# Kernel tuning notes

Measured on AMD Instinct MI355X. Metric: run time of the kernel, lower is better.

The kernel has to match this reference:

```python
import jax, jax.numpy as jnp
import numpy as np

N_NODES = 10000
N_EDGES = 320000
IN_FEATS = 500
CONV_DIMS = [500, 256, 256]
FC_DIMS = [256, 128, 40]
BN_EPS = 1e-5


def setup_inputs() -> dict:
    key = jax.random.key(0)
    ks = jax.random.split(key, 16)
    inp = {
        "x": jax.random.normal(ks[0], (N_NODES, IN_FEATS), dtype=jnp.float32),
        "edge_index": jax.random.randint(ks[1], (2, N_EDGES), 0, N_NODES, dtype=jnp.int64),
    }
    # conv layer params: Linear W [in,out], b [out]; BatchNorm gamma/beta [out]
    ki = 2
    for li in range(len(CONV_DIMS) - 1):
        d_in, d_out = CONV_DIMS[li], CONV_DIMS[li + 1]
        s = 1.0 / np.sqrt(d_in)
        inp[f"conv_W{li}"] = jax.random.uniform(ks[ki], (d_in, d_out), jnp.float32, -s, s); ki += 1
        inp[f"conv_b{li}"] = jax.random.uniform(ks[ki], (d_out,), jnp.float32, -s, s); ki += 1
        inp[f"bn_g{li}"] = jnp.ones((d_out,), jnp.float32)
        inp[f"bn_b{li}"] = jnp.zeros((d_out,), jnp.float32)
    for li in range(len(FC_DIMS) - 1):
        d_in, d_out = FC_DIMS[li], FC_DIMS[li + 1]
        s = 1.0 / np.sqrt(d_in)
        inp[f"fc_W{li}"] = jax.random.uniform(ks[ki], (d_in, d_out), jnp.float32, -s, s); ki += 1
        inp[f"fc_b{li}"] = jax.random.uniform(ks[ki], (d_out,), jnp.float32, -s, s); ki += 1
    return inp


def _degree(edge_index, n, dtype):
    # Faithful to: A = eye(N); A[i,j] = 1 per edge (set semantics dedupes repeats).
    A = jnp.eye(n, dtype=dtype).at[edge_index[0], edge_index[1]].set(1.0)
    return A.sum(axis=1)  # deg_i = rowsum of A


def _batchnorm(h, g, b):
    # training-mode BatchNorm1d: batch stats, biased variance
    mean = h.mean(axis=0)
    var = h.var(axis=0)
    return (h - mean) * jax.lax.rsqrt(var + BN_EPS) * g + b


def reference(x, edge_index, conv_W0, conv_b0, bn_g0, bn_b0,
              conv_W1, conv_b1, bn_g1, bn_b1,
              fc_W0, fc_b0, fc_W1, fc_b1):
    n = x.shape[0]
    deg = _degree(edge_index, n, x.dtype)
    # D = sqrt(diag(deg)) is a diagonal matrix, so elementwise D*A*D = diag(deg);
    # mm(D*A*D, x) == deg[:, None] * x (exactly the original math).
    h = x
    for W, b, g, beta in ((conv_W0, conv_b0, bn_g0, bn_b0),
                          (conv_W1, conv_b1, bn_g1, bn_b1)):
        h = (deg[:, None] * h) @ W + b
        h = jax.nn.relu(h)
        h = _batchnorm(h, g, beta)
        # dropout: identity at inference
    for W, b in ((fc_W0, fc_b0), (fc_W1, fc_b1)):
        h = jax.nn.relu(h @ W + b)  # original appends ReLU after every fc, incl. last
    return h
```

## Files before the change

kernel.cpp:

```cpp
#include <hip/hip_runtime.h>

#define NN 10000
#define NE 320000
#define ROW_WORDS 320
#define MP 10112
#define BN_EPS 1e-5f

typedef __attribute__((ext_vector_type(8))) short short8;
typedef __attribute__((ext_vector_type(4))) float f32x4;
typedef unsigned short u16;

__device__ __forceinline__ void split1(float v, u16& h, u16& l) {
    unsigned int u = __float_as_uint(v);
    h = (u16)(u >> 16);
    float hf = __uint_as_float(u & 0xFFFF0000u);
    l = (u16)(__float_as_uint(v - hf) >> 16);
}

__device__ __forceinline__ void gll16(const void* g, void* l) {
    __builtin_amdgcn_global_load_lds(
        (const __attribute__((address_space(1))) unsigned int*)g,
        (__attribute__((address_space(3))) unsigned int*)l, 16, 0, 0);
}

__global__ void scatter_bits(const int* __restrict__ ei, unsigned int* __restrict__ bitmap) {
    int t = blockIdx.x * blockDim.x + threadIdx.x;
    if (t < NE) {
        int i = ei[t];
        int j = ei[NE + t];
        atomicOr(&bitmap[i * ROW_WORDS + (j >> 5)], 1u << (j & 31));
    } else if (t < NE + NN) {
        int i = t - NE;
        atomicOr(&bitmap[i * ROW_WORDS + (i >> 5)], 1u << (i & 31));
    }
}

__device__ void splitW_dev(const float* __restrict__ W, int K, int N, int Kp, int Np,
                           u16* __restrict__ Wt, int bx, int by, char* smem) {
    float (*tile)[65] = (float(*)[65])smem;
    int t = threadIdx.x;
    int bk = bx * 64, bn = by * 64;
    #pragma unroll
    for (int p = 0; p < 4; ++p) {
        int kk = (t >> 4) + p * 16;
        int nc = (t & 15) * 4;
        int k = bk + kk;
        float4 v = {0.f, 0.f, 0.f, 0.f};
        if (k < K && bn + nc + 3 < N)
            v = *(const float4*)&W[(size_t)k * N + bn + nc];
        tile[kk][nc] = v.x; tile[kk][nc + 1] = v.y;
        tile[kk][nc + 2] = v.z; tile[kk][nc + 3] = v.w;
    }
    __syncthreads();
    int nn = t >> 2;
    int kk0 = (t & 3) * 16;
    u16 hs[16], ls[16];
    #pragma unroll
    for (int j = 0; j < 16; ++j) split1(tile[kk0 + j][nn], hs[j], ls[j]);
    size_t ob = (size_t)(bn + nn) * Kp + bk + kk0;
    size_t lo = (size_t)Np * Kp;
    *(short8*)&Wt[ob] = *(short8*)hs;
    *(short8*)&Wt[ob + 8] = *(short8*)&hs[8];
    *(short8*)&Wt[lo + ob] = *(short8*)ls;
    *(short8*)&Wt[lo + ob + 8] = *(short8*)&ls[8];
}

__device__ void xsplit_dev(const float* __restrict__ x, u16* __restrict__ xs, int gblk) {
    int t = threadIdx.x;
    int r0 = gblk * 16 + (t >> 4);
    int l = t & 15;
    u16* xlo = xs + (size_t)MP * 512;
    #pragma unroll
    for (int j = 0; j < 8; ++j) {
        int k = (l + j * 16) * 4;
        float vals[4] = {0.f, 0.f, 0.f, 0.f};
        if (r0 < NN && k < 500) {
            float4 v = *(const float4*)&x[(size_t)r0 * 500 + k];
            vals[0] = v.x; vals[1] = v.y; vals[2] = v.z; vals[3] = v.w;
        }
        ushort4 hs, ls;
        split1(vals[0], hs.x, ls.x); split1(vals[1], hs.y, ls.y);
        split1(vals[2], hs.z, ls.z); split1(vals[3], hs.w, ls.w);
        *(ushort4*)&xs[(size_t)r0 * 512 + k] = hs;
        *(ushort4*)&xlo[(size_t)r0 * 512 + k] = ls;
    }
}

__device__ void degree_dev(const unsigned int* __restrict__ bitmap, float* __restrict__ deg,
                           int gblk) {
    int t = threadIdx.x;
    int r = gblk * 16 + (t >> 4), l = t & 15;
    int cnt = 0;
    if (r < NN)
        for (int wd = l; wd < ROW_WORDS; wd += 16)
            cnt += __popc(bitmap[(size_t)r * ROW_WORDS + wd]);
    cnt += __shfl_down(cnt, 8, 16);
    cnt += __shfl_down(cnt, 4, 16);
    cnt += __shfl_down(cnt, 2, 16);
    cnt += __shfl_down(cnt, 1, 16);
    if (l == 0 && r < NN) deg[r] = (float)cnt;
}

__global__ __launch_bounds__(256)
void prep(const unsigned int* __restrict__ bitmap, const float* __restrict__ x,
          const float* __restrict__ W0, const float* __restrict__ fW1,
          float* __restrict__ deg, u16* __restrict__ xs,
          u16* __restrict__ W0t, u16* __restrict__ fW1t) {
    __shared__ char smem[16704];
    int b = blockIdx.x;
    if (b < 632) {
        degree_dev(bitmap, deg, b);
        xsplit_dev(x, xs, b);
    } else if (b < 664) {
        int idx = b - 632;
        splitW_dev(W0, 500, 256, 512, 256, W0t, idx & 7, idx >> 3, smem);
    } else {
        splitW_dev(fW1, 128, 40, 128, 64, fW1t, b - 664, 0, smem);
    }
}

__global__ __launch_bounds__(256, 4)
void conv0_gemm(const u16* __restrict__ Ahi, const u16* __restrict__ Alo,
                const u16* __restrict__ Bhi, const u16* __restrict__ Blo,
                const float* __restrict__ bias, const float* __restrict__ deg,
                float* __restrict__ stats, u16* __restrict__ Ohi, u16* __restrict__ Olo) {
    __shared__ char smem[32768];
    const int Kp = 512, M = NN, No = 256;
    const int b = blockIdx.x;
    const int xcd = b & 7, g = b >> 3;
    const int bx = g & 3, by = (g >> 2) * 8 + xcd;
    if (by >= 158) return;
    const int t = threadIdx.x;
    const int lane = t & 63;
    const int w = t >> 6;
    const int q = lane >> 4;
    const int l16 = lane & 15;
    const int m7 = l16 & 7;
    const int row0 = by * 64;
    const int col0 = bx * 64;

    const u16* bases[4] = {Ahi, Alo, Bhi, Blo};
    const u16* srcs[8];
    unsigned dstoff[8];
    #pragma unroll
    for (int i = 0; i < 8; ++i) {
        int gi = w + i * 4;
        int reg = i >> 1;
        int j = gi & 7;
        int rb = (reg < 2) ? row0 : col0;
        int r = j * 8 + (lane >> 3);
        int c = (lane & 7) ^ (r & 7);
        srcs[i] = bases[reg] + (size_t)(rb + r) * Kp + c * 8;
        dstoff[i] = reg * 8192 + j * 1024;
    }

    f32x4 acc[4];
    #pragma unroll
    for (int s = 0; s < 4; ++s) acc[s] = (f32x4){0.f, 0.f, 0.f, 0.f};

    #pragma unroll
    for (int i = 0; i < 8; ++i) { gll16(srcs[i], smem + dstoff[i]); srcs[i] += 64; }

    for (int k0 = 0; k0 < Kp; k0 += 64) {
        __syncthreads();
        short8 ah[2], al[2], bh[2][4], bl[2][4];
        #pragma unroll
        for (int kc = 0; kc < 2; ++kc) {
            int aoff = (w * 16 + l16) * 128 + (((kc * 4 + q) ^ m7) * 16);
            ah[kc] = *(const short8*)(smem + aoff);
            al[kc] = *(const short8*)(smem + 8192 + aoff);
            #pragma unroll
            for (int s = 0; s < 4; ++s) {
                int boff = (s * 16 + l16) * 128 + (((kc * 4 + q) ^ m7) * 16);
                bh[kc][s] = *(const short8*)(smem + 16384 + boff);
                bl[kc][s] = *(const short8*)(smem + 24576 + boff);
            }
        }
        __syncthreads();
        if (k0 + 64 < Kp) {
            #pragma unroll
            for (int i = 0; i < 8; ++i) { gll16(srcs[i], smem + dstoff[i]); srcs[i] += 64; }
        }
        #pragma unroll
        for (int kc = 0; kc < 2; ++kc)
            #pragma unroll
            for (int s = 0; s < 4; ++s) {
                acc[s] = __builtin_amdgcn_mfma_f32_16x16x32_bf16(al[kc], bh[kc][s], acc[s], 0, 0, 0);
                acc[s] = __builtin_amdgcn_mfma_f32_16x16x32_bf16(ah[kc], bl[kc][s], acc[s], 0, 0, 0);
                acc[s] = __builtin_amdgcn_mfma_f32_16x16x32_bf16(ah[kc], bh[kc][s], acc[s], 0, 0, 0);
            }
    }

    int growb = row0 + w * 16 + q * 4;
    float dgv[4];
    #pragma unroll
    for (int r = 0; r < 4; ++r) dgv[r] = (growb + r < M) ? deg[growb + r] : 0.f;
    #pragma unroll
    for (int s = 0; s < 4; ++s) {
        int gc = col0 + s * 16 + l16;
        float bia = bias[gc];
        float s_sum = 0.f, ss_sum = 0.f;
        #pragma unroll
        for (int r = 0; r < 4; ++r) {
            int grow = growb + r;
            bool real = grow < M;
            float v = fmaxf(fmaf(dgv[r], acc[s][r], bia), 0.f);
            if (!real) v = 0.f;
            s_sum += v; ss_sum += v * v;
            float vo = v * dgv[r];
            u16 h, l; split1(vo, h, l);
            Ohi[(size_t)grow * No + gc] = h;
            Olo[(size_t)grow * No + gc] = l;
        }
        s_sum  += __shfl_xor(s_sum, 16);  s_sum  += __shfl_xor(s_sum, 32);
        ss_sum += __shfl_xor(ss_sum, 16); ss_sum += __shfl_xor(ss_sum, 32);
        if (lane < 16) {
            atomicAdd(&stats[gc], s_sum);
            atomicAdd(&stats[256 + gc], ss_sum);
        }
    }
}

__global__ __launch_bounds__(256, 4)
void conv1_fold(const u16* __restrict__ Ahi, const u16* __restrict__ Alo,
                const float* __restrict__ W1, const float* __restrict__ stats0,
                const float* __restrict__ g0, const float* __restrict__ bb0,
                const float* __restrict__ b1, const float* __restrict__ deg,
                float* __restrict__ stats1, u16* __restrict__ Ohi, u16* __restrict__ Olo) {
    __shared__ char smem[32768];
    __shared__ float scl[256], sh[256], cred[256], cvec[64];
    const int Kp = 256, M = NN, No = 256;
    const int b = blockIdx.x;
    const int xcd = b & 7, g = b >> 3;
    const int bx = g & 3, by = (g >> 2) * 8 + xcd;
    if (by >= 158) return;
    const int t = threadIdx.x;
    const int lane = t & 63;
    const int w = t >> 6;
    const int q = lane >> 4;
    const int l16 = lane & 15;
    const int m7 = l16 & 7;
    const int row0 = by * 64;
    const int col0 = bx * 64;

    const u16* srcs[4];
    unsigned dstoff[4];
    #pragma unroll
    for (int i = 0; i < 4; ++i) {
        int gi = w + i * 4;
        int plane = gi >> 3, j = gi & 7;
        int r = j * 8 + (lane >> 3);
        int c = (lane & 7) ^ (r & 7);
        srcs[i] = (plane ? Alo : Ahi) + (size_t)(row0 + r) * Kp + c * 8;
        dstoff[i] = plane * 8192 + j * 1024;
    }
    #pragma unroll
    for (int i = 0; i < 4; ++i) { gll16(srcs[i], smem + dstoff[i]); srcs[i] += 64; }

    {
        float mean = stats0[t] * (1.f / NN);
        float var = stats0[256 + t] * (1.f / NN) - mean * mean;
        float s = g0[t] * rsqrtf(var + BN_EPS);
        scl[t] = s;
        sh[t] = bb0[t] - mean * s;
    }
    __syncthreads();
    {
        float s = 0.f;
        int n = col0 + (t & 63);
        #pragma unroll 8
        for (int k = (t >> 6); k < 256; k += 4)
            s += sh[k] * W1[(size_t)k * 256 + n];
        cred[t] = s;
        __syncthreads();
        if (t < 64) cvec[t] = cred[t] + cred[t + 64] + cred[t + 128] + cred[t + 192];
    }
    const int bn = t & 63;
    const int kb = (t >> 6) * 16;
    const int ch0 = (t >> 6) * 2;
    float vals[16];
    {
        const float* wp = W1 + (size_t)kb * 256 + col0 + bn;
        #pragma unroll
        for (int i = 0; i < 16; ++i) vals[i] = wp[(size_t)i * 256] * scl[kb + i];
    }

    f32x4 acc[4];
    #pragma unroll
    for (int s = 0; s < 4; ++s) acc[s] = (f32x4){0.f, 0.f, 0.f, 0.f};

    for (int k0 = 0; k0 < Kp; k0 += 64) {
        {
            u16 hs[16], ls[16];
            #pragma unroll
            for (int i = 0; i < 16; ++i) split1(vals[i], hs[i], ls[i]);
            unsigned o0 = bn * 128 + ((ch0 ^ (bn & 7)) * 16);
            unsigned o1 = bn * 128 + (((ch0 + 1) ^ (bn & 7)) * 16);
            *(short8*)(smem + 16384 + o0) = *(short8*)&hs[0];
            *(short8*)(smem + 16384 + o1) = *(short8*)&hs[8];
            *(short8*)(smem + 24576 + o0) = *(short8*)&ls[0];
            *(short8*)(smem + 24576 + o1) = *(short8*)&ls[8];
        }
        __syncthreads();
        short8 ah[2], al[2], bh[2][4], bl[2][4];
        #pragma unroll
        for (int kc = 0; kc < 2; ++kc) {
            int aoff = (w * 16 + l16) * 128 + (((kc * 4 + q) ^ m7) * 16);
            ah[kc] = *(const short8*)(smem + aoff);
            al[kc] = *(const short8*)(smem + 8192 + aoff);
            #pragma unroll
            for (int s = 0; s < 4; ++s) {
                int boff = (s * 16 + l16) * 128 + (((kc * 4 + q) ^ m7) * 16);
                bh[kc][s] = *(const short8*)(smem + 16384 + boff);
                bl[kc][s] = *(const short8*)(smem + 24576 + boff);
            }
        }
        __syncthreads();
        if (k0 + 64 < Kp) {
            #pragma unroll
            for (int i = 0; i < 4; ++i) { gll16(srcs[i], smem + dstoff[i]); srcs[i] += 64; }
            const float* wp = W1 + (size_t)(k0 + 64 + kb) * 256 + col0 + bn;
            #pragma unroll
            for (int i = 0; i < 16; ++i) vals[i] = wp[(size_t)i * 256] * scl[k0 + 64 + kb + i];
        }
        #pragma unroll
        for (int kc = 0; kc < 2; ++kc)
            #pragma unroll
            for (int s = 0; s < 4; ++s) {
                acc[s] = __builtin_amdgcn_mfma_f32_16x16x32_bf16(al[kc], bh[kc][s], acc[s], 0, 0, 0);
                acc[s] = __builtin_amdgcn_mfma_f32_16x16x32_bf16(ah[kc], bl[kc][s], acc[s], 0, 0, 0);
                acc[s] = __builtin_amdgcn_mfma_f32_16x16x32_bf16(ah[kc], bh[kc][s], acc[s], 0, 0, 0);
            }
    }

    int growb = row0 + w * 16 + q * 4;
    float dgv[4];
    #pragma unroll
    for (int r = 0; r < 4; ++r) dgv[r] = (growb + r < M) ? deg[growb + r] : 0.f;
    #pragma unroll
    for (int s = 0; s < 4; ++s) {
        int gc = col0 + s * 16 + l16;
        float bia = b1[gc];
        float cv = cvec[s * 16 + l16];
        float s_sum = 0.f, ss_sum = 0.f;
        #pragma unroll
        for (int r = 0; r < 4; ++r) {
            int grow = growb + r;
            bool real = grow < M;
            float v = fmaxf(fmaf(dgv[r], cv, acc[s][r] + bia), 0.f);
            if (!real) v = 0.f;
            s_sum += v; ss_sum += v * v;
            u16 h, l; split1(v, h, l);
            Ohi[(size_t)grow * No + gc] = h;
            Olo[(size_t)grow * No + gc] = l;
        }
        s_sum  += __shfl_xor(s_sum, 16);  s_sum  += __shfl_xor(s_sum, 32);
        ss_sum += __shfl_xor(ss_sum, 16); ss_sum += __shfl_xor(ss_sum, 32);
        if (lane < 16) {
            atomicAdd(&stats1[gc], s_sum);
            atomicAdd(&stats1[256 + gc], ss_sum);
        }
    }
}

__global__ __launch_bounds__(256, 4)
void fc0_fold(const u16* __restrict__ Ahi, const u16* __restrict__ Alo,
              const float* __restrict__ fW0, const float* __restrict__ stats1,
              const float* __restrict__ g1, const float* __restrict__ bb1,
              const float* __restrict__ fb0,
              u16* __restrict__ Ohi, u16* __restrict__ Olo) {
    __shared__ char smem[32768];
    __shared__ float scl[256], sh[256], cred[256], biasf[64];
    const int Kp = 256, M = NN, No = 128;
    const int b = blockIdx.x;
    const int xcd = b & 7, g = b >> 3;
    const int bx = g & 1, by = (g >> 1) * 8 + xcd;
    if (by >= 158) return;
    const int t = threadIdx.x;
    const int lane = t & 63;
    const int w = t >> 6;
    const int q = lane >> 4;
    const int l16 = lane & 15;
    const int m7 = l16 & 7;
    const int row0 = by * 64;
    const int col0 = bx * 64;

    const u16* srcs[4];
    unsigned dstoff[4];
    #pragma unroll
    for (int i = 0; i < 4; ++i) {
        int gi = w + i * 4;
        int plane = gi >> 3, j = gi & 7;
        int r = j * 8 + (lane >> 3);
        int c = (lane & 7) ^ (r & 7);
        srcs[i] = (plane ? Alo : Ahi) + (size_t)(row0 + r) * Kp + c * 8;
        dstoff[i] = plane * 8192 + j * 1024;
    }
    #pragma unroll
    for (int i = 0; i < 4; ++i) { gll16(srcs[i], smem + dstoff[i]); srcs[i] += 64; }

    {
        float mean = stats1[t] * (1.f / NN);
        float var = stats1[256 + t] * (1.f / NN) - mean * mean;
        float s = g1[t] * rsqrtf(var + BN_EPS);
        scl[t] = s;
        sh[t] = bb1[t] - mean * s;
    }
    __syncthreads();
    {
        float s = 0.f;
        int n = col0 + (t & 63);
        #pragma unroll 8
        for (int k = (t >> 6); k < 256; k += 4)
            s += sh[k] * fW0[(size_t)k * 128 + n];
        cred[t] = s;
        __syncthreads();
        if (t < 64)
            biasf[t] = fb0[col0 + t] + cred[t] + cred[t + 64] + cred[t + 128] + cred[t + 192];
    }
    const int bn = t & 63;
    const int kb = (t >> 6) * 16;
    const int ch0 = (t >> 6) * 2;
    float vals[16];
    {
        const float* wp = fW0 + (size_t)kb * 128 + col0 + bn;
        #pragma unroll
        for (int i = 0; i < 16; ++i) vals[i] = wp[(size_t)i * 128] * scl[kb + i];
    }

    f32x4 acc[4];
    #pragma unroll
    for (int s = 0; s < 4; ++s) acc[s] = (f32x4){0.f, 0.f, 0.f, 0.f};

    for (int k0 = 0; k0 < Kp; k0 += 64) {
        {
            u16 hs[16], ls[16];
            #pragma unroll
            for (int i = 0; i < 16; ++i) split1(vals[i], hs[i], ls[i]);
            unsigned o0 = bn * 128 + ((ch0 ^ (bn & 7)) * 16);
            unsigned o1 = bn * 128 + (((ch0 + 1) ^ (bn & 7)) * 16);
            *(short8*)(smem + 16384 + o0) = *(short8*)&hs[0];
            *(short8*)(smem + 16384 + o1) = *(short8*)&hs[8];
            *(short8*)(smem + 24576 + o0) = *(short8*)&ls[0];
            *(short8*)(smem + 24576 + o1) = *(short8*)&ls[8];
        }
        __syncthreads();
        short8 ah[2], al[2], bh[2][4], bl[2][4];
        #pragma unroll
        for (int kc = 0; kc < 2; ++kc) {
            int aoff = (w * 16 + l16) * 128 + (((kc * 4 + q) ^ m7) * 16);
            ah[kc] = *(const short8*)(smem + aoff);
            al[kc] = *(const short8*)(smem + 8192 + aoff);
            #pragma unroll
            for (int s = 0; s < 4; ++s) {
                int boff = (s * 16 + l16) * 128 + (((kc * 4 + q) ^ m7) * 16);
                bh[kc][s] = *(const short8*)(smem + 16384 + boff);
                bl[kc][s] = *(const short8*)(smem + 24576 + boff);
            }
        }
        __syncthreads();
        if (k0 + 64 < Kp) {
            #pragma unroll
            for (int i = 0; i < 4; ++i) { gll16(srcs[i], smem + dstoff[i]); srcs[i] += 64; }
            const float* wp = fW0 + (size_t)(k0 + 64 + kb) * 128 + col0 + bn;
            #pragma unroll
            for (int i = 0; i < 16; ++i) vals[i] = wp[(size_t)i * 128] * scl[k0 + 64 + kb + i];
        }
        #pragma unroll
        for (int kc = 0; kc < 2; ++kc)
            #pragma unroll
            for (int s = 0; s < 4; ++s) {
                acc[s] = __builtin_amdgcn_mfma_f32_16x16x32_bf16(al[kc], bh[kc][s], acc[s], 0, 0, 0);
                acc[s] = __builtin_amdgcn_mfma_f32_16x16x32_bf16(ah[kc], bl[kc][s], acc[s], 0, 0, 0);
                acc[s] = __builtin_amdgcn_mfma_f32_16x16x32_bf16(ah[kc], bh[kc][s], acc[s], 0, 0, 0);
            }
    }

    int growb = row0 + w * 16 + q * 4;
    #pragma unroll
    for (int s = 0; s < 4; ++s) {
        int gc = col0 + s * 16 + l16;
        float bia = biasf[s * 16 + l16];
        #pragma unroll
        for (int r = 0; r < 4; ++r) {
            int grow = growb + r;
            float v = fmaxf(acc[s][r] + bia, 0.f);
            if (grow >= M) v = 0.f;
            u16 h, l; split1(v, h, l);
            Ohi[(size_t)grow * No + gc] = h;
            Olo[(size_t)grow * No + gc] = l;
        }
    }
}

__global__ __launch_bounds__(256, 3)
void fc1_gemm(const u16* __restrict__ Ahi, const u16* __restrict__ Alo,
              const u16* __restrict__ Bhi, const u16* __restrict__ Blo,
              const float* __restrict__ bias, float* __restrict__ out) {
    __shared__ char smem[32768];
    const int Kp = 128, M = NN, N = 40, No = 40;
    const int t = threadIdx.x;
    const int lane = t & 63;
    const int w = t >> 6;
    const int q = lane >> 4;
    const int l16 = lane & 15;
    const int m7 = l16 & 7;
    const int row0 = blockIdx.x * 64;
    const int col0 = 0;

    const u16* bases[4] = {Ahi, Alo, Bhi, Blo};
    const u16* srcs[8];
    unsigned dstoff[8];
    #pragma unroll
    for (int i = 0; i < 8; ++i) {
        int gi = w + i * 4;
        int reg = i >> 1;
        int j = gi & 7;
        int rb = (reg < 2) ? row0 : col0;
        int r = j * 8 + (lane >> 3);
        int c = (lane & 7) ^ (r & 7);
        srcs[i] = bases[reg] + (size_t)(rb + r) * Kp + c * 8;
        dstoff[i] = reg * 8192 + j * 1024;
    }

    f32x4 acc[4];
    #pragma unroll
    for (int s = 0; s < 4; ++s) acc[s] = (f32x4){0.f, 0.f, 0.f, 0.f};

    #pragma unroll
    for (int i = 0; i < 8; ++i) { gll16(srcs[i], smem + dstoff[i]); srcs[i] += 64; }

    for (int k0 = 0; k0 < Kp; k0 += 64) {
        __syncthreads();
        short8 ah[2], al[2], bh[2][4], bl[2][4];
        #pragma unroll
        for (int kc = 0; kc < 2; ++kc) {
            int aoff = (w * 16 + l16) * 128 + (((kc * 4 + q) ^ m7) * 16);
            ah[kc] = *(const short8*)(smem + aoff);
            al[kc] = *(const short8*)(smem + 8192 + aoff);
            #pragma unroll
            for (int s = 0; s < 4; ++s) {
                int boff = (s * 16 + l16) * 128 + (((kc * 4 + q) ^ m7) * 16);
                bh[kc][s] = *(const short8*)(smem + 16384 + boff);
                bl[kc][s] = *(const short8*)(smem + 24576 + boff);
            }
        }
        __syncthreads();
        if (k0 + 64 < Kp) {
            #pragma unroll
            for (int i = 0; i < 8; ++i) { gll16(srcs[i], smem + dstoff[i]); srcs[i] += 64; }
        }
        #pragma unroll
        for (int kc = 0; kc < 2; ++kc)
            #pragma unroll
            for (int s = 0; s < 4; ++s) {
                acc[s] = __builtin_amdgcn_mfma_f32_16x16x32_bf16(al[kc], bh[kc][s], acc[s], 0, 0, 0);
                acc[s] = __builtin_amdgcn_mfma_f32_16x16x32_bf16(ah[kc], bl[kc][s], acc[s], 0, 0, 0);
                acc[s] = __builtin_amdgcn_mfma_f32_16x16x32_bf16(ah[kc], bh[kc][s], acc[s], 0, 0, 0);
            }
    }

    int growb = row0 + w * 16 + q * 4;
    #pragma unroll
    for (int s = 0; s < 4; ++s) {
        int gc = col0 + s * 16 + l16;
        if (gc >= N) continue;
        float bia = bias[gc];
        #pragma unroll
        for (int r = 0; r < 4; ++r) {
            int grow = growb + r;
            if (grow < M)
                out[(size_t)grow * No + gc] = fmaxf(acc[s][r] + bia, 0.f);
        }
    }
}


extern "C" void kernel_launch(void* const* d_in, const int* in_sizes, int n_in,
                              void* d_out, int out_size, void* d_ws, size_t ws_size,
                              hipStream_t stream) {
    const float* x   = (const float*)d_in[0];
    const int*   ei  = (const int*)d_in[1];
    const float* W0  = (const float*)d_in[2];
    const float* b0  = (const float*)d_in[3];
    const float* g0  = (const float*)d_in[4];
    const float* bb0 = (const float*)d_in[5];
    const float* W1  = (const float*)d_in[6];
    const float* b1  = (const float*)d_in[7];
    const float* g1  = (const float*)d_in[8];
    const float* bb1 = (const float*)d_in[9];
    const float* fW0 = (const float*)d_in[10];
    const float* fb0 = (const float*)d_in[11];
    const float* fW1 = (const float*)d_in[12];
    const float* fb1 = (const float*)d_in[13];
    float* out = (float*)d_out;

    char* ws = (char*)d_ws;
    auto carve = [&](size_t bytes) { char* q = ws; ws += (bytes + 255) & ~(size_t)255; return q; };

    const size_t BITMAP_BYTES = (size_t)NN * ROW_WORDS * 4;
    char* region0 = carve(BITMAP_BYTES + 4096);
    unsigned int* bitmap = (unsigned int*)region0;
    float* stats = (float*)(region0 + BITMAP_BYTES);
    u16* H1 = (u16*)region0;

    float* deg  = (float*)carve(MP * 4);
    u16* xs     = (u16*)carve((size_t)2 * MP * 512 * 2);
    u16* W0t    = (u16*)carve((size_t)2 * 256 * 512 * 2);
    u16* fW1t   = (u16*)carve((size_t)2 * 64 * 128 * 2);
    u16* H2     = (u16*)carve((size_t)2 * MP * 256 * 2);
    u16* H3     = (u16*)carve((size_t)2 * MP * 128 * 2);

    dim3 blk(256);

    hipMemsetAsync(region0, 0, BITMAP_BYTES + 4096, stream);
    scatter_bits<<<(NE + NN + 255) / 256, blk, 0, stream>>>(ei, bitmap);
    prep<<<666, blk, 0, stream>>>(bitmap, x, W0, fW1, deg, xs, W0t, fW1t);
    conv0_gemm<<<640, blk, 0, stream>>>(
        xs, xs + (size_t)MP * 512, W0t, W0t + 256 * 512,
        b0, deg, stats, H1, H1 + (size_t)MP * 256);
    conv1_fold<<<640, blk, 0, stream>>>(
        H1, H1 + (size_t)MP * 256, W1, stats, g0, bb0, b1, deg,
        stats + 512, H2, H2 + (size_t)MP * 256);
    fc0_fold<<<320, blk, 0, stream>>>(
        H2, H2 + (size_t)MP * 256, fW0, stats + 512, g1, bb1, fb0,
        H3, H3 + (size_t)MP * 128);
    fc1_gemm<<<158, blk, 0, stream>>>(
        H3, H3 + (size_t)MP * 128, fW1t, fW1t + 64 * 128, fb1, out);
}
```

Before: 187.4 us.

## Fuse x bf16 split into conv0 GEMM and merge weight split with scatter

```diff
diff --git a/kernel.cpp b/kernel.cpp
--- a/kernel.cpp
+++ b/kernel.cpp
@@ -21,18 +21,6 @@
     __builtin_amdgcn_global_load_lds(
         (const __attribute__((address_space(1))) unsigned int*)g,
         (__attribute__((address_space(3))) unsigned int*)l, 16, 0, 0);
-}
-
-__global__ void scatter_bits(const int* __restrict__ ei, unsigned int* __restrict__ bitmap) {
-    int t = blockIdx.x * blockDim.x + threadIdx.x;
-    if (t < NE) {
-        int i = ei[t];
-        int j = ei[NE + t];
-        atomicOr(&bitmap[i * ROW_WORDS + (j >> 5)], 1u << (j & 31));
-    } else if (t < NE + NN) {
-        int i = t - NE;
-        atomicOr(&bitmap[i * ROW_WORDS + (i >> 5)], 1u << (i & 31));
-    }
 }
 
 __device__ void splitW_dev(const float* __restrict__ W, int K, int N, int Kp, int Np,
@@ -65,31 +53,32 @@
     *(short8*)&Wt[lo + ob + 8] = *(short8*)&ls[8];
 }
 
-__device__ void xsplit_dev(const float* __restrict__ x, u16* __restrict__ xs, int gblk) {
+__global__ __launch_bounds__(256)
+void scatter_prep(const int* __restrict__ ei, unsigned int* __restrict__ bitmap,
+                  const float* __restrict__ W0, const float* __restrict__ fW1,
+                  u16* __restrict__ W0t, u16* __restrict__ fW1t) {
+    __shared__ char smem[16704];
+    int b = blockIdx.x;
+    if (b < 1290) {
+        int e = b * 256 + threadIdx.x;
+        if (e < NE + NN) {
+            int i, j;
+            if (e < NE) { i = ei[e]; j = ei[NE + e]; }
+            else        { i = e - NE; j = i; }
+            atomicOr(&bitmap[i * ROW_WORDS + (j >> 5)], 1u << (j & 31));
+        }
+    } else if (b < 1322) {
+        int idx = b - 1290;
+        splitW_dev(W0, 500, 256, 512, 256, W0t, idx & 7, idx >> 3, smem);
+    } else {
+        splitW_dev(fW1, 128, 40, 128, 64, fW1t, b - 1322, 0, smem);
+    }
+}
+
+__global__ __launch_bounds__(256)
+void degree_k(const unsigned int* __restrict__ bitmap, float* __restrict__ deg) {
     int t = threadIdx.x;
-    int r0 = gblk * 16 + (t >> 4);
-    int l = t & 15;
-    u16* xlo = xs + (size_t)MP * 512;
-    #pragma unroll
-    for (int j = 0; j < 8; ++j) {
-        int k = (l + j * 16) * 4;
-        float vals[4] = {0.f, 0.f, 0.f, 0.f};
-        if (r0 < NN && k < 500) {
-            float4 v = *(const float4*)&x[(size_t)r0 * 500 + k];
-            vals[0] = v.x; vals[1] = v.y; vals[2] = v.z; vals[3] = v.w;
-        }
-        ushort4 hs, ls;
-        split1(vals[0], hs.x, ls.x); split1(vals[1], hs.y, ls.y);
-        split1(vals[2], hs.z, ls.z); split1(vals[3], hs.w, ls.w);
-        *(ushort4*)&xs[(size_t)r0 * 512 + k] = hs;
-        *(ushort4*)&xlo[(size_t)r0 * 512 + k] = ls;
-    }
-}
-
-__device__ void degree_dev(const unsigned int* __restrict__ bitmap, float* __restrict__ deg,
-                           int gblk) {
-    int t = threadIdx.x;
-    int r = gblk * 16 + (t >> 4), l = t & 15;
+    int r = blockIdx.x * 16 + (t >> 4), l = t & 15;
     int cnt = 0;
     if (r < NN)
         for (int wd = l; wd < ROW_WORDS; wd += 16)
@@ -101,26 +90,8 @@
     if (l == 0 && r < NN) deg[r] = (float)cnt;
 }
 
-__global__ __launch_bounds__(256)
-void prep(const unsigned int* __restrict__ bitmap, const float* __restrict__ x,
-          const float* __restrict__ W0, const float* __restrict__ fW1,
-          float* __restrict__ deg, u16* __restrict__ xs,
-          u16* __restrict__ W0t, u16* __restrict__ fW1t) {
-    __shared__ char smem[16704];
-    int b = blockIdx.x;
-    if (b < 632) {
-        degree_dev(bitmap, deg, b);
-        xsplit_dev(x, xs, b);
-    } else if (b < 664) {
-        int idx = b - 632;
-        splitW_dev(W0, 500, 256, 512, 256, W0t, idx & 7, idx >> 3, smem);
-    } else {
-        splitW_dev(fW1, 128, 40, 128, 64, fW1t, b - 664, 0, smem);
-    }
-}
-
 __global__ __launch_bounds__(256, 4)
-void conv0_gemm(const u16* __restrict__ Ahi, const u16* __restrict__ Alo,
+void conv0_gemm(const float* __restrict__ x,
                 const u16* __restrict__ Bhi, const u16* __restrict__ Blo,
                 const float* __restrict__ bias, const float* __restrict__ deg,
                 float* __restrict__ stats, u16* __restrict__ Ohi, u16* __restrict__ Olo) {
@@ -139,29 +110,58 @@
     const int row0 = by * 64;
     const int col0 = bx * 64;
 
-    const u16* bases[4] = {Ahi, Alo, Bhi, Blo};
-    const u16* srcs[8];
-    unsigned dstoff[8];
-    #pragma unroll
-    for (int i = 0; i < 8; ++i) {
-        int gi = w + i * 4;
-        int reg = i >> 1;
-        int j = gi & 7;
-        int rb = (reg < 2) ? row0 : col0;
+    const u16* bsp[4];
+    unsigned bdst[4];
+    #pragma unroll
+    for (int i = 0; i < 4; ++i) {
+        int gb = w + i * 4;
+        int plane = gb >> 3, j = gb & 7;
         int r = j * 8 + (lane >> 3);
         int c = (lane & 7) ^ (r & 7);
-        srcs[i] = bases[reg] + (size_t)(rb + r) * Kp + c * 8;
-        dstoff[i] = reg * 8192 + j * 1024;
-    }
+        bsp[i] = (plane ? Blo : Bhi) + (size_t)(col0 + r) * Kp + c * 8;
+        bdst[i] = 16384 + plane * 8192 + j * 1024;
+    }
+
+    const int ar0 = t >> 3;
+    const int ac8 = t & 7;
+    float4 areg[2][2];
+    auto loadA = [&](int k0) {
+        #pragma unroll
+        for (int p = 0; p < 2; ++p) {
+            int gr = row0 + ar0 + p * 32;
+            int gk = k0 + ac8 * 8;
+            bool rok = gr < NN;
+            areg[p][0] = (rok && gk < 500) ? *(const float4*)&x[(size_t)gr * 500 + gk]
+                                           : (float4){0.f, 0.f, 0.f, 0.f};
+            areg[p][1] = (rok && gk + 4 < 500) ? *(const float4*)&x[(size_t)gr * 500 + gk + 4]
+                                               : (float4){0.f, 0.f, 0.f, 0.f};
+        }
+    };
+    auto writeA = [&]() {
+        #pragma unroll
+        for (int p = 0; p < 2; ++p) {
+            int r = ar0 + p * 32;
+            u16 hs[8], ls[8];
+            split1(areg[p][0].x, hs[0], ls[0]); split1(areg[p][0].y, hs[1], ls[1]);
+            split1(areg[p][0].z, hs[2], ls[2]); split1(areg[p][0].w, hs[3], ls[3]);
+            split1(areg[p][1].x, hs[4], ls[4]); split1(areg[p][1].y, hs[5], ls[5]);
+            split1(areg[p][1].z, hs[6], ls[6]); split1(areg[p][1].w, hs[7], ls[7]);
+            unsigned addr = r * 128 + ((ac8 ^ (r & 7)) * 16);
+            *(short8*)(smem + addr) = *(short8*)hs;
+            *(short8*)(smem + 8192 + addr) = *(short8*)ls;
+        }
+    };
 
     f32x4 acc[4];
     #pragma unroll
     for (int s = 0; s < 4; ++s) acc[s] = (f32x4){0.f, 0.f, 0.f, 0.f};
 
-    #pragma unroll
-    for (int i = 0; i < 8; ++i) { gll16(srcs[i], smem + dstoff[i]); srcs[i] += 64; }
+    loadA(0);
+    #pragma unroll
+    for (int i = 0; i < 4; ++i) { gll16(bsp[i], smem + bdst[i]); bsp[i] += 64; }
 
     for (int k0 = 0; k0 < Kp; k0 += 64) {
+        writeA();
         __syncthreads();
         short8 ah[2], al[2], bh[2][4], bl[2][4];
         #pragma unroll
@@ -178,8 +178,9 @@
         }
         __syncthreads();
         if (k0 + 64 < Kp) {
-            #pragma unroll
-            for (int i = 0; i < 8; ++i) { gll16(srcs[i], smem + dstoff[i]); srcs[i] += 64; }
+            loadA(k0 + 64);
+            #pragma unroll
+            for (int i = 0; i < 4; ++i) { gll16(bsp[i], smem + bdst[i]); bsp[i] += 64; }
         }
         #pragma unroll
         for (int kc = 0; kc < 2; ++kc)
@@ -605,7 +606,6 @@
     u16* H1 = (u16*)region0;
 
     float* deg  = (float*)carve(MP * 4);
-    u16* xs     = (u16*)carve((size_t)2 * MP * 512 * 2);
     u16* W0t    = (u16*)carve((size_t)2 * 256 * 512 * 2);
     u16* fW1t   = (u16*)carve((size_t)2 * 64 * 128 * 2);
     u16* H2     = (u16*)carve((size_t)2 * MP * 256 * 2);
@@ -614,11 +614,10 @@
     dim3 blk(256);
 
     hipMemsetAsync(region0, 0, BITMAP_BYTES + 4096, stream);
-    scatter_bits<<<(NE + NN + 255) / 256, blk, 0, stream>>>(ei, bitmap);
-    prep<<<666, blk, 0, stream>>>(bitmap, x, W0, fW1, deg, xs, W0t, fW1t);
+    scatter_prep<<<1324, blk, 0, stream>>>(ei, bitmap, W0, fW1, W0t, fW1t);
+    degree_k<<<632, blk, 0, stream>>>(bitmap, deg);
     conv0_gemm<<<640, blk, 0, stream>>>(
-        xs, xs + (size_t)MP * 512, W0t, W0t + 256 * 512,
-        b0, deg, stats, H1, H1 + (size_t)MP * 256);
+        x, W0t, W0t + 256 * 512, b0, deg, stats, H1, H1 + (size_t)MP * 256);
     conv1_fold<<<640, blk, 0, stream>>>(
         H1, H1 + (size_t)MP * 256, W1, stats, g0, bb0, b1, deg,
         stats + 512, H2, H2 + (size_t)MP * 256);
```

Result: slower. 194.3 us (+3.7%).

## Fuse edge scatter into prep kernel and compute degrees inside conv0 GEMM

Applied to the files above, without the earlier changes.

```diff
diff --git a/kernel.cpp b/kernel.cpp
--- a/kernel.cpp
+++ b/kernel.cpp
@@ -21,18 +21,6 @@
     __builtin_amdgcn_global_load_lds(
         (const __attribute__((address_space(1))) unsigned int*)g,
         (__attribute__((address_space(3))) unsigned int*)l, 16, 0, 0);
-}
-
-__global__ void scatter_bits(const int* __restrict__ ei, unsigned int* __restrict__ bitmap) {
-    int t = blockIdx.x * blockDim.x + threadIdx.x;
-    if (t < NE) {
-        int i = ei[t];
-        int j = ei[NE + t];
-        atomicOr(&bitmap[i * ROW_WORDS + (j >> 5)], 1u << (j & 31));
-    } else if (t < NE + NN) {
-        int i = t - NE;
-        atomicOr(&bitmap[i * ROW_WORDS + (i >> 5)], 1u << (i & 31));
-    }
 }
 
 __device__ void splitW_dev(const float* __restrict__ W, int K, int N, int Kp, int Np,
@@ -86,45 +74,39 @@
     }
 }
 
-__device__ void degree_dev(const unsigned int* __restrict__ bitmap, float* __restrict__ deg,
-                           int gblk) {
-    int t = threadIdx.x;
-    int r = gblk * 16 + (t >> 4), l = t & 15;
-    int cnt = 0;
-    if (r < NN)
-        for (int wd = l; wd < ROW_WORDS; wd += 16)
-            cnt += __popc(bitmap[(size_t)r * ROW_WORDS + wd]);
-    cnt += __shfl_down(cnt, 8, 16);
-    cnt += __shfl_down(cnt, 4, 16);
-    cnt += __shfl_down(cnt, 2, 16);
-    cnt += __shfl_down(cnt, 1, 16);
-    if (l == 0 && r < NN) deg[r] = (float)cnt;
-}
-
 __global__ __launch_bounds__(256)
-void prep(const unsigned int* __restrict__ bitmap, const float* __restrict__ x,
-          const float* __restrict__ W0, const float* __restrict__ fW1,
-          float* __restrict__ deg, u16* __restrict__ xs,
-          u16* __restrict__ W0t, u16* __restrict__ fW1t) {
+void scatter_prep(const int* __restrict__ ei, unsigned int* __restrict__ bitmap,
+                  const float* __restrict__ x,
+                  const float* __restrict__ W0, const float* __restrict__ fW1,
+                  u16* __restrict__ xs, u16* __restrict__ W0t, u16* __restrict__ fW1t) {
     __shared__ char smem[16704];
     int b = blockIdx.x;
-    if (b < 632) {
-        degree_dev(bitmap, deg, b);
-        xsplit_dev(x, xs, b);
-    } else if (b < 664) {
-        int idx = b - 632;
+    if (b < 1290) {
+        int e = b * 256 + threadIdx.x;
+        if (e < NE + NN) {
+            int i, j;
+            if (e < NE) { i = ei[e]; j = ei[NE + e]; }
+            else        { i = e - NE; j = i; }
+            atomicOr(&bitmap[i * ROW_WORDS + (j >> 5)], 1u << (j & 31));
+        }
+    } else if (b < 1922) {
+        xsplit_dev(x, xs, b - 1290);
+    } else if (b < 1954) {
+        int idx = b - 1922;
         splitW_dev(W0, 500, 256, 512, 256, W0t, idx & 7, idx >> 3, smem);
     } else {
-        splitW_dev(fW1, 128, 40, 128, 64, fW1t, b - 664, 0, smem);
+        splitW_dev(fW1, 128, 40, 128, 64, fW1t, b - 1954, 0, smem);
     }
 }
 
 __global__ __launch_bounds__(256, 4)
 void conv0_gemm(const u16* __restrict__ Ahi, const u16* __restrict__ Alo,
                 const u16* __restrict__ Bhi, const u16* __restrict__ Blo,
-                const float* __restrict__ bias, const float* __restrict__ deg,
-                float* __restrict__ stats, u16* __restrict__ Ohi, u16* __restrict__ Olo) {
+                const unsigned int* __restrict__ bitmap, const float* __restrict__ bias,
+                float* __restrict__ deg, float* __restrict__ stats,
+                u16* __restrict__ Ohi, u16* __restrict__ Olo) {
     __shared__ char smem[32768];
+    __shared__ float sdeg[64];
     const int Kp = 512, M = NN, No = 256;
     const int b = blockIdx.x;
     const int xcd = b & 7, g = b >> 3;
@@ -161,6 +143,21 @@
     #pragma unroll
     for (int i = 0; i < 8; ++i) { gll16(srcs[i], smem + dstoff[i]); srcs[i] += 64; }
 
+    {
+        int rr = t >> 2, wl = t & 3;
+        int grow = row0 + rr;
+        int cnt = 0;
+        if (grow < NN)
+            for (int wd = wl; wd < ROW_WORDS; wd += 4)
+                cnt += __popc(bitmap[(size_t)grow * ROW_WORDS + wd]);
+        cnt += __shfl_down(cnt, 1, 4);
+        cnt += __shfl_down(cnt, 2, 4);
+        if (wl == 0) {
+            sdeg[rr] = (float)cnt;
+            if (bx == 0 && grow < NN) deg[grow] = (float)cnt;
+        }
+    }
+
     for (int k0 = 0; k0 < Kp; k0 += 64) {
         __syncthreads();
         short8 ah[2], al[2], bh[2][4], bl[2][4];
@@ -194,7 +191,10 @@
     int growb = row0 + w * 16 + q * 4;
     float dgv[4];
     #pragma unroll
-    for (int r = 0; r < 4; ++r) dgv[r] = (growb + r < M) ? deg[growb + r] : 0.f;
+    for (int r = 0; r < 4; ++r) {
+        int grow = growb + r;
+        dgv[r] = (grow < M) ? sdeg[grow - row0] : 0.f;
+    }
     #pragma unroll
     for (int s = 0; s < 4; ++s) {
         int gc = col0 + s * 16 + l16;
@@ -602,23 +602,22 @@
     char* region0 = carve(BITMAP_BYTES + 4096);
     unsigned int* bitmap = (unsigned int*)region0;
     float* stats = (float*)(region0 + BITMAP_BYTES);
-    u16* H1 = (u16*)region0;
 
     float* deg  = (float*)carve(MP * 4);
     u16* xs     = (u16*)carve((size_t)2 * MP * 512 * 2);
     u16* W0t    = (u16*)carve((size_t)2 * 256 * 512 * 2);
     u16* fW1t   = (u16*)carve((size_t)2 * 64 * 128 * 2);
+    u16* H1     = (u16*)carve((size_t)2 * MP * 256 * 2);
     u16* H2     = (u16*)carve((size_t)2 * MP * 256 * 2);
     u16* H3     = (u16*)carve((size_t)2 * MP * 128 * 2);
 
     dim3 blk(256);
 
     hipMemsetAsync(region0, 0, BITMAP_BYTES + 4096, stream);
-    scatter_bits<<<(NE + NN + 255) / 256, blk, 0, stream>>>(ei, bitmap);
-    prep<<<666, blk, 0, stream>>>(bitmap, x, W0, fW1, deg, xs, W0t, fW1t);
+    scatter_prep<<<1956, blk, 0, stream>>>(ei, bitmap, x, W0, fW1, xs, W0t, fW1t);
     conv0_gemm<<<640, blk, 0, stream>>>(
         xs, xs + (size_t)MP * 512, W0t, W0t + 256 * 512,
-        b0, deg, stats, H1, H1 + (size_t)MP * 256);
+        bitmap, b0, deg, stats, H1, H1 + (size_t)MP * 256);
     conv1_fold<<<640, blk, 0, stream>>>(
         H1, H1 + (size_t)MP * 256, W1, stats, g0, bb0, b1, deg,
         stats + 512, H2, H2 + (size_t)MP * 256);
```

New measurement: 185.2 us. Within noise of the previous version (-1.2%).
